# Kernel optimization log

Hardware: AMD Instinct MI355X
Metric: run time of the kernel (lower is better)

The kernel has to match this reference:

```python
import jax, jax.numpy as jnp
import numpy as np

V = 50000      # vocab_size
E = 512        # embed_size
H = 512        # hidden_size
B = 128        # batch
S = 256        # encoder seq len
MAX_OOVS = 12


def setup_inputs() -> dict:
    key = jax.random.key(0)
    ks = jax.random.split(key, 18)
    s = 0.05
    embed_table = jax.random.normal(ks[4], (V, E), jnp.float32) * s
    embed_table = embed_table.at[0].set(0.0)  # padding_idx=0
    return {
        'input_idx':   jax.random.randint(ks[0], (B,), 0, V),
        'encoded':     jax.random.normal(ks[1], (B, S, H), jnp.float32),
        'encoded_idx': jax.random.randint(ks[2], (B, S), 0, V),
        'prev_state':  jax.random.normal(ks[3], (B, H), jnp.float32),
        'weighted':    jnp.zeros((B, 1, H), jnp.float32),
        'embed_table': embed_table,
        'Ws_w':    jax.random.normal(ks[5], (H, H), jnp.float32) * s,
        'Ws_b':    jnp.zeros((H,), jnp.float32),
        'gru_Wih': jax.random.normal(ks[6], (3 * H, E + H), jnp.float32) * s,
        'gru_Whh': jax.random.normal(ks[7], (3 * H, H), jnp.float32) * s,
        'gru_bih': jnp.zeros((3 * H,), jnp.float32),
        'gru_bhh': jnp.zeros((3 * H,), jnp.float32),
        'attn_W':  jax.random.normal(ks[8], (H, 2 * H), jnp.float32) * s,
        'attn_b':  jnp.zeros((H,), jnp.float32),
        'attn_v':  jax.random.normal(ks[9], (H,), jnp.float32) * s,
        'Wo_w':    jax.random.normal(ks[10], (V, 2 * H), jnp.float32) * s,
        'Wo_b':    jnp.zeros((V,), jnp.float32),
        'Wc_w':    jax.random.normal(ks[11], (2 * H, H), jnp.float32) * s,
        'Wc_b':    jnp.zeros((2 * H,), jnp.float32),
    }


def copy_decoder_fwd(input_idx, encoded, encoded_idx, prev_state, weighted,
                     embed_table, Ws_w, Ws_b, gru_Wih, gru_Whh, gru_bih, gru_bhh,
                     attn_W, attn_b, attn_v, Wo_w, Wo_b, Wc_w, Wc_b):
    b, seq, hidden = encoded.shape
    vocab = Wo_w.shape[0]
    dt = encoded.dtype

    # order == 0 branch: project prev_state, zero the weighted context
    prev = prev_state @ Ws_w.T + Ws_b                      # (b, h)
    wtd = jnp.zeros((b, hidden), dt)                       # (b, h)

    # GRU single step (PyTorch gate layout: r, z, n)
    x = jnp.concatenate([embed_table[input_idx], wtd], axis=1)  # (b, e+h)
    gi = x @ gru_Wih.T + gru_bih                           # (b, 3h)
    gh = prev @ gru_Whh.T + gru_bhh                        # (b, 3h)
    i_r, i_z, i_n = jnp.split(gi, 3, axis=1)
    h_r, h_z, h_n = jnp.split(gh, 3, axis=1)
    r = jax.nn.sigmoid(i_r + h_r)
    z = jax.nn.sigmoid(i_z + h_z)
    n = jnp.tanh(i_n + r * h_n)
    state = (1.0 - z) * n + z * prev                       # (b, h), == rnn_output

    # 'concat' attention: softmax_seq(v . tanh(W[h; enc] + b))
    h_exp = jnp.broadcast_to(state[:, None, :], (b, seq, hidden))
    energy = jnp.tanh(jnp.concatenate([h_exp, encoded], axis=-1) @ attn_W.T + attn_b)
    attn_w = jax.nn.softmax(energy @ attn_v, axis=1)       # (b, seq)
    context = jnp.einsum('bs,bsh->bh', attn_w, encoded)    # (b, h)

    # generation scores
    score_g = jnp.concatenate([state, context], axis=1) @ Wo_w.T + Wo_b  # (b, V)

    # copy scores
    sc = jnp.tanh(encoded @ Wc_w.T + Wc_b)                 # (b, seq, 2h)
    score_c = jnp.einsum('bsk,bk->bs', sc, jnp.concatenate([state, context], axis=1))
    score_c = score_c + jnp.where(encoded_idx == 0, -1000.0, 0.0).astype(dt)

    # joint softmax over vocab + seq
    probs = jax.nn.softmax(jnp.concatenate([score_g, score_c], axis=1), axis=1)
    prob_g = probs[:, :vocab]                              # (b, V)
    prob_c = probs[:, vocab:]                              # (b, seq)
    prob_c_given = prob_c / jnp.sum(prob_c)                # global-scalar normalization (faithful)

    # pad generation probs with small oov mass
    vext = vocab + MAX_OOVS
    prob_g_ext = jnp.concatenate(
        [prob_g, jnp.full((b, MAX_OOVS), 1e-4, dt)], axis=1)  # (b, V+oov)

    # copy -> vocab scatter-add (replaces dense one-hot + bmm)
    batch_ids = jnp.broadcast_to(jnp.arange(b)[:, None], (b, seq))
    prob_c_to_g = jnp.zeros((b, vext), dt).at[batch_ids, encoded_idx].add(prob_c)

    out = (prob_g_ext + prob_c_to_g)[:, None, :]           # (b, 1, V+oov)

    # positions in source equal to the current input token
    ind = (encoded_idx == input_idx[:, None]).astype(dt)   # (b, seq)
    ssum = ind.sum(axis=1, keepdims=True)
    ind = jnp.where(ssum > 1.0, ind / ssum, ind)
    attn2 = prob_c_given * ind                             # (b, seq)
    weighted_new = jnp.einsum('bs,bsh->bh', attn2, encoded)[:, None, :]  # (b, 1, h)

    return out, state, weighted_new


def reference(input_idx, encoded, encoded_idx, prev_state, weighted,
              embed_table, Ws_w, Ws_b, gru_Wih, gru_Whh, gru_bih, gru_bhh,
              attn_W, attn_b, attn_v, Wo_w, Wo_b, Wc_w, Wc_b):
    return copy_decoder_fwd(input_idx, encoded, encoded_idx, prev_state, weighted,
                            embed_table, Ws_w, Ws_b, gru_Wih, gru_Whh, gru_bih, gru_bhh,
                            attn_W, attn_b, attn_v, Wo_w, Wo_b, Wc_w, Wc_b)
```

## Files before the change

### kernel.cpp

```cpp
#include <hip/hip_runtime.h>
#include <hip/hip_bf16.h>
#include <math.h>

#define BB 128
#define SS 256
#define HH 512
#define VV 50000
#define VEXT 50012

typedef __bf16 bf16x8 __attribute__((ext_vector_type(8)));
typedef float f32x4 __attribute__((ext_vector_type(4)));

__device__ __forceinline__ float fast_tanh(float x) {
  float e = __expf(2.0f * x);
  return 1.0f - 2.0f / (e + 1.0f);
}
__device__ __forceinline__ float fast_sigmoid(float x) {
  return 1.0f / (1.0f + __expf(-x));
}
__device__ __forceinline__ bf16x8 cvt8(const float* p) {
  float4 a = *(const float4*)p;
  float4 b = *(const float4*)(p + 4);
  bf16x8 r;
  r[0] = (__bf16)a.x; r[1] = (__bf16)a.y; r[2] = (__bf16)a.z; r[3] = (__bf16)a.w;
  r[4] = (__bf16)b.x; r[5] = (__bf16)b.y; r[6] = (__bf16)b.z; r[7] = (__bf16)b.w;
  return r;
}

__global__ void k_pack_w(const float* __restrict__ src, int ldw, int coff, int icount,
                         __hip_bfloat16* __restrict__ dst) {
  int i = blockIdx.x * 256 + threadIdx.x;
  if (i >= icount) return;
  int l = i & 63, ks = (i >> 6) & 15, tile = i >> 10;
  int m = l & 15, q = l >> 4;
  const float* p = src + (size_t)(tile * 16 + m) * ldw + coff + ks * 32 + q * 8;
  *(bf16x8*)(dst + (size_t)i * 8) = cvt8(p);
}

__global__ void k_pack_enc(const float* __restrict__ enc, __hip_bfloat16* __restrict__ epk) {
  int i = blockIdx.x * 256 + threadIdx.x;
  int l = i & 63, ks = (i >> 6) & 15, st = (i >> 10) & 15, b = i >> 14;
  int m = l & 15, q = l >> 4;
  const float* p = enc + ((size_t)b * SS + st * 16 + m) * HH + ks * 32 + q * 8;
  *(bf16x8*)(epk + (size_t)i * 8) = cvt8(p);
}

template <int LDB, bool GATHER>
__global__ __launch_bounds__(256, 2) void k_gemm_bt(
    const float* __restrict__ A, const float* __restrict__ B,
    const float* __restrict__ bias, float* __restrict__ C, int ldc,
    const int* __restrict__ gidx) {
  __shared__ __hip_bfloat16 ylds[128 * 72];
  const int t = threadIdx.x;
  const int l = t & 63, w = t >> 6;
  const int m = l & 15, q = l >> 4;
  const int n = blockIdx.x * 64 + w * 16 + m;
  const float* wrow = B + (size_t)n * LDB;
  f32x4 acc[8];
#pragma unroll
  for (int mt = 0; mt < 8; ++mt) acc[mt] = (f32x4){0.f, 0.f, 0.f, 0.f};

  for (int kt = 0; kt < 512; kt += 64) {
    __syncthreads();
#pragma unroll
    for (int i = 0; i < 8; ++i) {
      int f = t + i * 256;
      int row = f >> 4, c4 = f & 15;
      const float* arow;
      if (GATHER)
        arow = A + (size_t)gidx[row] * 512;
      else
        arow = A + (size_t)row * 512;
      float4 v = *(const float4*)(arow + kt + c4 * 4);
      __hip_bfloat16* d = ylds + row * 72 + c4 * 4;
      d[0] = __float2bfloat16(v.x); d[1] = __float2bfloat16(v.y);
      d[2] = __float2bfloat16(v.z); d[3] = __float2bfloat16(v.w);
    }
    __syncthreads();
#pragma unroll
    for (int ksl = 0; ksl < 2; ++ksl) {
      bf16x8 bfr = cvt8(wrow + kt + ksl * 32 + q * 8);
#pragma unroll
      for (int mt = 0; mt < 8; ++mt) {
        bf16x8 af = *(const bf16x8*)(ylds + (mt * 16 + m) * 72 + ksl * 32 + q * 8);
        acc[mt] = __builtin_amdgcn_mfma_f32_16x16x32_bf16(af, bfr, acc[mt], 0, 0, 0);
      }
    }
  }
  float bv = bias[n];
#pragma unroll
  for (int mt = 0; mt < 8; ++mt) {
#pragma unroll
    for (int r = 0; r < 4; ++r) {
      int rowm = mt * 16 + q * 4 + r;
      C[(size_t)rowm * ldc + n] = acc[mt][r] + bv;
    }
  }
}

__global__ void k_gates(const float* __restrict__ gi, const float* __restrict__ gh,
                        const float* __restrict__ prevv, float* __restrict__ state,
                        float* __restrict__ state_out) {
  int i = blockIdx.x * 256 + threadIdx.x;
  int b = i >> 9, h = i & 511;
  const float* gib = gi + (size_t)b * 1536;
  const float* ghb = gh + (size_t)b * 1536;
  float ir = gib[h], iz = gib[512 + h], inn = gib[1024 + h];
  float hr = ghb[h], hz = ghb[512 + h], hn = ghb[1024 + h];
  float r = fast_sigmoid(ir + hr);
  float z = fast_sigmoid(iz + hz);
  float n = fast_tanh(inn + r * hn);
  float st = (1.f - z) * n + z * prevv[i];
  state[i] = st;
  state_out[i] = st;
}

template <int NTOT, int MODE>
__global__ __launch_bounds__(256, 3) void k_fused(
    const __hip_bfloat16* __restrict__ epack, const __hip_bfloat16* __restrict__ wpk,
    const float* __restrict__ biasA, const float* __restrict__ multA,
    const int* __restrict__ enc_idx, float* __restrict__ out) {
  const int b = blockIdx.x, s0 = blockIdx.y * 32, t = threadIdx.x;
  const int l = t & 63, w = t >> 6;
  const int wm = w & 1, wn = w >> 1;
  const int m = l & 15, q = l >> 4;
  __shared__ float bias_l[NTOT];
  __shared__ float mult_l[NTOT];
  __shared__ float red[2][32];
  const float* bias_base = (MODE == 0) ? biasA + (size_t)b * HH : biasA;
  const float* mult_base = (MODE == 0) ? multA : multA + (size_t)b * 1024;
  for (int i = t; i < NTOT; i += 256) {
    bias_l[i] = bias_base[i];
    mult_l[i] = mult_base[i];
  }
  const int st = blockIdx.y * 2 + wm;
  const __hip_bfloat16* ep = epack + ((size_t)(b * 16 + st) * 16) * 512 + (size_t)l * 8;
  bf16x8 afr[16];
#pragma unroll
  for (int ks = 0; ks < 16; ++ks) afr[ks] = *(const bf16x8*)(ep + ks * 512);
  __syncthreads();

  float part[4] = {0.f, 0.f, 0.f, 0.f};
  for (int nb = 0; nb < NTOT; nb += 32) {
    const __hip_bfloat16* wp = wpk + ((size_t)((nb >> 4) + wn) * 16) * 512 + (size_t)l * 8;
    bf16x8 bfr[16];
#pragma unroll
    for (int ks = 0; ks < 16; ++ks) bfr[ks] = *(const bf16x8*)(wp + ks * 512);
    f32x4 a0 = {0.f, 0.f, 0.f, 0.f}, a1 = a0, a2 = a0, a3 = a0;
#pragma unroll
    for (int j = 0; j < 4; ++j) {
      a0 = __builtin_amdgcn_mfma_f32_16x16x32_bf16(afr[j], bfr[j], a0, 0, 0, 0);
      a1 = __builtin_amdgcn_mfma_f32_16x16x32_bf16(afr[4 + j], bfr[4 + j], a1, 0, 0, 0);
      a2 = __builtin_amdgcn_mfma_f32_16x16x32_bf16(afr[8 + j], bfr[8 + j], a2, 0, 0, 0);
      a3 = __builtin_amdgcn_mfma_f32_16x16x32_bf16(afr[12 + j], bfr[12 + j], a3, 0, 0, 0);
    }
    f32x4 acc = (a0 + a1) + (a2 + a3);
    const int n = nb + wn * 16 + m;
    float bias = bias_l[n];
    float mul = mult_l[n];
#pragma unroll
    for (int r = 0; r < 4; ++r) part[r] += fast_tanh(acc[r] + bias) * mul;
  }
#pragma unroll
  for (int r = 0; r < 4; ++r) {
    part[r] += __shfl_xor(part[r], 1, 64);
    part[r] += __shfl_xor(part[r], 2, 64);
    part[r] += __shfl_xor(part[r], 4, 64);
    part[r] += __shfl_xor(part[r], 8, 64);
  }
  if (m == 0) {
#pragma unroll
    for (int r = 0; r < 4; ++r) red[wn][wm * 16 + q * 4 + r] = part[r];
  }
  __syncthreads();
  if (t < 32) {
    float v = red[0][t] + red[1][t];
    int s = s0 + t;
    if (MODE == 1 && enc_idx[b * SS + s] == 0) v -= 1000.0f;
    out[b * SS + s] = v;
  }
}

__global__ __launch_bounds__(256, 2) void k_score_g_mfma(
    const float* __restrict__ y, const float* __restrict__ Wo_w,
    const float* __restrict__ Wo_b, float* __restrict__ sg) {
  __shared__ __hip_bfloat16 ylds[128 * 72];
  const int t = threadIdx.x;
  const int l = t & 63, w = t >> 6;
  const int m = l & 15, q = l >> 4;
  const int nb = blockIdx.x * 64;
  const int n = nb + w * 16 + m;
  const int n_ld = (n < VV) ? n : (VV - 1);
  const float* wrow = Wo_w + (size_t)n_ld * 1024;
  f32x4 acc[8];
#pragma unroll
  for (int mt = 0; mt < 8; ++mt) acc[mt] = (f32x4){0.f, 0.f, 0.f, 0.f};

  for (int kt = 0; kt < 1024; kt += 64) {
    __syncthreads();
#pragma unroll
    for (int i = 0; i < 8; ++i) {
      int f = t + i * 256;
      int row = f >> 4, c4 = f & 15;
      float4 v = *(const float4*)(y + (size_t)row * 1024 + kt + c4 * 4);
      __hip_bfloat16* d = ylds + row * 72 + c4 * 4;
      d[0] = __float2bfloat16(v.x); d[1] = __float2bfloat16(v.y);
      d[2] = __float2bfloat16(v.z); d[3] = __float2bfloat16(v.w);
    }
    __syncthreads();
#pragma unroll
    for (int ksl = 0; ksl < 2; ++ksl) {
      bf16x8 bfr = cvt8(wrow + kt + ksl * 32 + q * 8);
#pragma unroll
      for (int mt = 0; mt < 8; ++mt) {
        bf16x8 af = *(const bf16x8*)(ylds + (mt * 16 + m) * 72 + ksl * 32 + q * 8);
        acc[mt] = __builtin_amdgcn_mfma_f32_16x16x32_bf16(af, bfr, acc[mt], 0, 0, 0);
      }
    }
  }
  if (n < VV) {
    float bias = Wo_b[n];
#pragma unroll
    for (int mt = 0; mt < 8; ++mt) {
#pragma unroll
      for (int r = 0; r < 4; ++r) {
        int rowm = mt * 16 + q * 4 + r;
        sg[(size_t)rowm * VV + n] = acc[mt][r] + bias;
      }
    }
  }
}

__global__ void k_attn_softmax(const float* __restrict__ score, float* __restrict__ aw) {
  const int b = blockIdx.x, t = threadIdx.x;
  __shared__ float rbuf[8];
  __shared__ float MS[2];
  float x = score[b * SS + t];
  float m = x;
  for (int off = 32; off > 0; off >>= 1) m = fmaxf(m, __shfl_xor(m, off, 64));
  if ((t & 63) == 0) rbuf[t >> 6] = m;
  __syncthreads();
  if (t == 0) MS[0] = fmaxf(fmaxf(rbuf[0], rbuf[1]), fmaxf(rbuf[2], rbuf[3]));
  __syncthreads();
  float e = __expf(x - MS[0]);
  float s = e;
  for (int off = 32; off > 0; off >>= 1) s += __shfl_xor(s, off, 64);
  if ((t & 63) == 0) rbuf[4 + (t >> 6)] = s;
  __syncthreads();
  if (t == 0) MS[1] = rbuf[4] + rbuf[5] + rbuf[6] + rbuf[7];
  __syncthreads();
  aw[b * SS + t] = e / MS[1];
}

__global__ void k_context(const float* __restrict__ aw, const float* __restrict__ enc,
                          const float* __restrict__ state, float* __restrict__ y) {
  const int b = blockIdx.x, hc = blockIdx.y, t = threadIdx.x;
  __shared__ float aws[SS];
  aws[t] = aw[b * SS + t];
  aws[t + 128] = aw[b * SS + t + 128];
  __syncthreads();
  int h = hc * 128 + t;
  float acc = 0.f;
  for (int s = 0; s < SS; ++s) acc += aws[s] * enc[((size_t)b * SS + s) * HH + h];
  y[(size_t)b * 1024 + HH + h] = acc;
  y[(size_t)b * 1024 + h] = state[b * HH + h];
}

__global__ void k_rowstat_part(const float* __restrict__ sg,
                               float* __restrict__ pmax, float* __restrict__ psum) {
  const int b = blockIdx.x, c = blockIdx.y, t = threadIdx.x;
  __shared__ float rbuf[8];
  __shared__ float MS[1];
  const float* row = sg + (size_t)b * VV;
  const int base = c * 6250, end = base + 6250;
  float m = -1e30f;
  for (int i = base + t; i < end; i += 256) m = fmaxf(m, row[i]);
  for (int off = 32; off > 0; off >>= 1) m = fmaxf(m, __shfl_xor(m, off, 64));
  if ((t & 63) == 0) rbuf[t >> 6] = m;
  __syncthreads();
  if (t == 0) MS[0] = fmaxf(fmaxf(rbuf[0], rbuf[1]), fmaxf(rbuf[2], rbuf[3]));
  __syncthreads();
  float M = MS[0];
  float s = 0.f;
  for (int i = base + t; i < end; i += 256) s += __expf(row[i] - M);
  for (int off = 32; off > 0; off >>= 1) s += __shfl_xor(s, off, 64);
  if ((t & 63) == 0) rbuf[4 + (t >> 6)] = s;
  __syncthreads();
  if (t == 0) {
    pmax[b * 8 + c] = M;
    psum[b * 8 + c] = rbuf[4] + rbuf[5] + rbuf[6] + rbuf[7];
  }
}

__global__ void k_rowstat_final(const float* __restrict__ pmax, const float* __restrict__ psum,
                                const float* __restrict__ sc,
                                float* __restrict__ rmax, float* __restrict__ rsum) {
  const int b = blockIdx.x, t = threadIdx.x;
  float m = -1e30f;
  if (t < 8) m = pmax[b * 8 + t];
  for (int i = t; i < SS; i += 64) m = fmaxf(m, sc[b * SS + i]);
  for (int off = 32; off > 0; off >>= 1) m = fmaxf(m, __shfl_xor(m, off, 64));
  float M = m;
  float s = 0.f;
  if (t < 8) s = psum[b * 8 + t] * __expf(pmax[b * 8 + t] - M);
  for (int i = t; i < SS; i += 64) s += __expf(sc[b * SS + i] - M);
  for (int off = 32; off > 0; off >>= 1) s += __shfl_xor(s, off, 64);
  if (t == 0) {
    rmax[b] = M;
    rsum[b] = s;
  }
}

__global__ void k_write_probg(const float* __restrict__ sg,
                              const float* __restrict__ rmax,
                              const float* __restrict__ rsum,
                              float* __restrict__ out) {
  int i = blockIdx.x * 256 + threadIdx.x;
  const int total = BB * VEXT;
  if (i >= total) return;
  int b = i / VEXT;
  int v = i - b * VEXT;
  float val;
  if (v < VV)
    val = __expf(sg[(size_t)b * VV + v] - rmax[b]) / rsum[b];
  else
    val = 1e-4f;
  out[i] = val;
}

__global__ void k_probc(const float* __restrict__ sc,
                        const int* __restrict__ enc_idx,
                        const float* __restrict__ rmax,
                        const float* __restrict__ rsum,
                        float* __restrict__ prob_c,
                        float* __restrict__ out,
                        float* __restrict__ pc_total) {
  const int b = blockIdx.x, t = threadIdx.x;
  __shared__ float rbuf[8];
  float pc = __expf(sc[b * SS + t] - rmax[b]) / rsum[b];
  prob_c[b * SS + t] = pc;
  atomicAdd(&out[(size_t)b * VEXT + enc_idx[b * SS + t]], pc);
  float s = pc;
  for (int off = 32; off > 0; off >>= 1) s += __shfl_down(s, off, 64);
  if ((t & 63) == 0) rbuf[t >> 6] = s;
  __syncthreads();
  if (t == 0) atomicAdd(pc_total, rbuf[0] + rbuf[1] + rbuf[2] + rbuf[3]);
}

__global__ void k_weighted(const int* __restrict__ enc_idx,
                           const int* __restrict__ input_idx,
                           const float* __restrict__ prob_c,
                           const float* __restrict__ pc_total,
                           const float* __restrict__ enc,
                           float* __restrict__ wout) {
  const int b = blockIdx.x, hc = blockIdx.y, t = threadIdx.x;
  __shared__ float f[SS];
  __shared__ float rb[2];
  const int idx_in = input_idx[b];
  int m0 = (enc_idx[b * SS + t] == idx_in) ? 1 : 0;
  int m1 = (enc_idx[b * SS + t + 128] == idx_in) ? 1 : 0;
  float lsum = (float)(m0 + m1);
  for (int off = 32; off > 0; off >>= 1) lsum += __shfl_xor(lsum, off, 64);
  if ((t & 63) == 0) rb[t >> 6] = lsum;
  __syncthreads();
  float tot = rb[0] + rb[1];
  float norm = (tot > 1.0f) ? 1.0f / tot : 1.0f;
  float inv_pct = 1.0f / pc_total[0];
  f[t] = m0 ? prob_c[b * SS + t] * inv_pct * norm : 0.f;
  f[t + 128] = m1 ? prob_c[b * SS + t + 128] * inv_pct * norm : 0.f;
  __syncthreads();
  int h = hc * 128 + t;
  float acc = 0.f;
  for (int s = 0; s < SS; ++s) acc += f[s] * enc[((size_t)b * SS + s) * HH + h];
  wout[b * HH + h] = acc;
}

extern "C" void kernel_launch(void* const* d_in, const int* in_sizes, int n_in,
                              void* d_out, int out_size, void* d_ws, size_t ws_size,
                              hipStream_t stream) {
  const int* input_idx = (const int*)d_in[0];
  const float* encoded = (const float*)d_in[1];
  const int* encoded_idx = (const int*)d_in[2];
  const float* prev_state = (const float*)d_in[3];
  const float* embed = (const float*)d_in[5];
  const float* Ws_w = (const float*)d_in[6];
  const float* Ws_b = (const float*)d_in[7];
  const float* gWih = (const float*)d_in[8];
  const float* gWhh = (const float*)d_in[9];
  const float* gbih = (const float*)d_in[10];
  const float* gbhh = (const float*)d_in[11];
  const float* attn_W = (const float*)d_in[12];
  const float* attn_b = (const float*)d_in[13];
  const float* attn_v = (const float*)d_in[14];
  const float* Wo_w = (const float*)d_in[15];
  const float* Wo_b = (const float*)d_in[16];
  const float* Wc_w = (const float*)d_in[17];
  const float* Wc_b = (const float*)d_in[18];

  float* out = (float*)d_out;
  float* out_state = out + (size_t)BB * VEXT;
  float* out_weighted = out_state + BB * HH;

  float* ws = (float*)d_ws;
  float* prevv = ws;
  float* state = prevv + BB * HH;
  float* hW = state + BB * HH;
  float* ascore = hW + BB * HH;
  float* aw = ascore + BB * SS;
  float* y = aw + BB * SS;
  float* sg = y + BB * 1024;
  float* sc = sg + (size_t)BB * VV;
  float* prob_c = sc + BB * SS;
  float* pmax = prob_c + BB * SS;
  float* psum = pmax + BB * 8;
  float* rmax = psum + BB * 8;
  float* rsum = rmax + BB;
  float* pc_total = rsum + BB;
  __hip_bfloat16* wc_bf = (__hip_bfloat16*)(pc_total + 64);
  __hip_bfloat16* wa_bf = wc_bf + (size_t)1024 * HH;
  __hip_bfloat16* epack = wa_bf + (size_t)512 * HH;

  float* gi = sg;
  float* gh = sg + BB * 1536;

  hipMemsetAsync(pc_total, 0, sizeof(float), stream);

  k_pack_w<<<256, 256, 0, stream>>>(Wc_w, 512, 0, 1024 * 64, wc_bf);
  k_pack_w<<<128, 256, 0, stream>>>(attn_W, 1024, 512, 512 * 64, wa_bf);
  k_pack_enc<<<8192, 256, 0, stream>>>(encoded, epack);

  k_gemm_bt<512, false><<<8, 256, 0, stream>>>(prev_state, Ws_w, Ws_b, prevv, 512, nullptr);
  k_gemm_bt<1024, true><<<24, 256, 0, stream>>>(embed, gWih, gbih, gi, 1536, input_idx);
  k_gemm_bt<512, false><<<24, 256, 0, stream>>>(prevv, gWhh, gbhh, gh, 1536, nullptr);
  k_gates<<<256, 256, 0, stream>>>(gi, gh, prevv, state, out_state);
  k_gemm_bt<1024, false><<<8, 256, 0, stream>>>(state, attn_W, attn_b, hW, 512, nullptr);

  k_fused<HH, 0><<<dim3(BB, 8), 256, 0, stream>>>(epack, wa_bf, hW, attn_v,
                                                  nullptr, ascore);
  k_attn_softmax<<<BB, 256, 0, stream>>>(ascore, aw);
  k_context<<<dim3(BB, 4), 128, 0, stream>>>(aw, encoded, state, y);

  k_score_g_mfma<<<(VV + 63) / 64, 256, 0, stream>>>(y, Wo_w, Wo_b, sg);
  k_fused<1024, 1><<<dim3(BB, 8), 256, 0, stream>>>(epack, wc_bf, Wc_b, y,
                                                    encoded_idx, sc);

  k_rowstat_part<<<dim3(BB, 8), 256, 0, stream>>>(sg, pmax, psum);
  k_rowstat_final<<<BB, 64, 0, stream>>>(pmax, psum, sc, rmax, rsum);
  k_write_probg<<<(BB * VEXT + 255) / 256, 256, 0, stream>>>(sg, rmax, rsum, out);
  k_probc<<<BB, 256, 0, stream>>>(sc, encoded_idx, rmax, rsum, prob_c, out, pc_total);
  k_weighted<<<dim3(BB, 4), 128, 0, stream>>>(encoded_idx, input_idx, prob_c, pc_total,
                                              encoded, out_weighted);
}
```

Measured before the change: 721.5 us.

## Fuse vocab softmax statistics into score GEMM epilogue and merge small kernels

The vocab score GEMM now computes per-block online max and sum-exp in its epilogue, which removes the separate row-stat pass over the 128x50000 score matrix. The final reduction merges 782 partials per row. y is pre-packed to bf16 in MFMA fragment order, so the score GEMM reads fragments directly instead of staging them through LDS with barriers. The attention softmax is fused with the context kernel, and the two GRU-input GEMMs share one launch. The context and weighted kernels use float4 loads with one block per batch row, trading fewer threads for wider loads.

```diff
diff --git a/kernel.cpp b/kernel.cpp
--- a/kernel.cpp
+++ b/kernel.cpp
@@ -7,6 +7,7 @@
 #define HH 512
 #define VV 50000
 #define VEXT 50012
+#define NBLK 782
 
 typedef __bf16 bf16x8 __attribute__((ext_vector_type(8)));
 typedef float f32x4 __attribute__((ext_vector_type(4)));
@@ -25,6 +26,11 @@
   r[0] = (__bf16)a.x; r[1] = (__bf16)a.y; r[2] = (__bf16)a.z; r[3] = (__bf16)a.w;
   r[4] = (__bf16)b.x; r[5] = (__bf16)b.y; r[6] = (__bf16)b.z; r[7] = (__bf16)b.w;
   return r;
+}
+__device__ __forceinline__ void omerge(float& M, float& S, float m2, float s2) {
+  float Mn = fmaxf(M, m2);
+  S = S * __expf(M - Mn) + s2 * __expf(m2 - Mn);
+  M = Mn;
 }
 
 __global__ void k_pack_w(const float* __restrict__ src, int ldw, int coff, int icount,
@@ -45,17 +51,23 @@
   *(bf16x8*)(epk + (size_t)i * 8) = cvt8(p);
 }
 
-template <int LDB, bool GATHER>
-__global__ __launch_bounds__(256, 2) void k_gemm_bt(
-    const float* __restrict__ A, const float* __restrict__ B,
-    const float* __restrict__ bias, float* __restrict__ C, int ldc,
-    const int* __restrict__ gidx) {
-  __shared__ __hip_bfloat16 ylds[128 * 72];
+__global__ void k_pack_y(const float* __restrict__ y, __hip_bfloat16* __restrict__ ypk) {
+  int i = blockIdx.x * 256 + threadIdx.x;
+  int l = i & 63, mt = (i >> 6) & 7, ks = i >> 9;
+  int m = l & 15, q = l >> 4;
+  const float* p = y + (size_t)(mt * 16 + m) * 1024 + ks * 32 + q * 8;
+  *(bf16x8*)(ypk + (size_t)i * 8) = cvt8(p);
+}
+
+__device__ __forceinline__ void gemm_body(
+    const float* __restrict__ A, const int* __restrict__ gidx, bool gather,
+    const float* __restrict__ B, int ldb, const float* __restrict__ bias,
+    float* __restrict__ C, int ldc, int blk, __hip_bfloat16* ylds) {
   const int t = threadIdx.x;
   const int l = t & 63, w = t >> 6;
   const int m = l & 15, q = l >> 4;
-  const int n = blockIdx.x * 64 + w * 16 + m;
-  const float* wrow = B + (size_t)n * LDB;
+  const int n = blk * 64 + w * 16 + m;
+  const float* wrow = B + (size_t)n * ldb;
   f32x4 acc[8];
 #pragma unroll
   for (int mt = 0; mt < 8; ++mt) acc[mt] = (f32x4){0.f, 0.f, 0.f, 0.f};
@@ -66,11 +78,7 @@
     for (int i = 0; i < 8; ++i) {
       int f = t + i * 256;
       int row = f >> 4, c4 = f & 15;
-      const float* arow;
-      if (GATHER)
-        arow = A + (size_t)gidx[row] * 512;
-      else
-        arow = A + (size_t)row * 512;
+      const float* arow = gather ? A + (size_t)gidx[row] * 512 : A + (size_t)row * 512;
       float4 v = *(const float4*)(arow + kt + c4 * 4);
       __hip_bfloat16* d = ylds + row * 72 + c4 * 4;
       d[0] = __float2bfloat16(v.x); d[1] = __float2bfloat16(v.y);
@@ -96,6 +104,25 @@
       C[(size_t)rowm * ldc + n] = acc[mt][r] + bv;
     }
   }
+}
+
+__global__ __launch_bounds__(256, 2) void k_gemm_pg(
+    const float* __restrict__ prev_state, const float* __restrict__ embed,
+    const int* __restrict__ gidx, const float* __restrict__ Ws_w,
+    const float* __restrict__ Ws_b, const float* __restrict__ gWih,
+    const float* __restrict__ gbih, float* __restrict__ prevv, float* __restrict__ gi) {
+  __shared__ __hip_bfloat16 ylds[128 * 72];
+  if (blockIdx.x < 8)
+    gemm_body(prev_state, nullptr, false, Ws_w, 512, Ws_b, prevv, 512, blockIdx.x, ylds);
+  else
+    gemm_body(embed, gidx, true, gWih, 1024, gbih, gi, 1536, blockIdx.x - 8, ylds);
+}
+
+__global__ __launch_bounds__(256, 2) void k_gemm_1(
+    const float* __restrict__ A, const float* __restrict__ B, int ldb,
+    const float* __restrict__ bias, float* __restrict__ C, int ldc) {
+  __shared__ __hip_bfloat16 ylds[128 * 72];
+  gemm_body(A, nullptr, false, B, ldb, bias, C, ldc, blockIdx.x, ylds);
 }
 
 __global__ void k_gates(const float* __restrict__ gi, const float* __restrict__ gh,
@@ -181,133 +208,119 @@
   }
 }
 
-__global__ __launch_bounds__(256, 2) void k_score_g_mfma(
-    const float* __restrict__ y, const float* __restrict__ Wo_w,
-    const float* __restrict__ Wo_b, float* __restrict__ sg) {
-  __shared__ __hip_bfloat16 ylds[128 * 72];
+__global__ __launch_bounds__(256, 2) void k_score_g2(
+    const __hip_bfloat16* __restrict__ ypk, const float* __restrict__ Wo_w,
+    const float* __restrict__ Wo_b, float* __restrict__ sg,
+    float* __restrict__ gmax, float* __restrict__ gsum) {
   const int t = threadIdx.x;
   const int l = t & 63, w = t >> 6;
   const int m = l & 15, q = l >> 4;
-  const int nb = blockIdx.x * 64;
-  const int n = nb + w * 16 + m;
+  const int n = blockIdx.x * 64 + w * 16 + m;
   const int n_ld = (n < VV) ? n : (VV - 1);
   const float* wrow = Wo_w + (size_t)n_ld * 1024;
   f32x4 acc[8];
 #pragma unroll
   for (int mt = 0; mt < 8; ++mt) acc[mt] = (f32x4){0.f, 0.f, 0.f, 0.f};
-
-  for (int kt = 0; kt < 1024; kt += 64) {
-    __syncthreads();
-#pragma unroll
-    for (int i = 0; i < 8; ++i) {
-      int f = t + i * 256;
-      int row = f >> 4, c4 = f & 15;
-      float4 v = *(const float4*)(y + (size_t)row * 1024 + kt + c4 * 4);
-      __hip_bfloat16* d = ylds + row * 72 + c4 * 4;
-      d[0] = __float2bfloat16(v.x); d[1] = __float2bfloat16(v.y);
-      d[2] = __float2bfloat16(v.z); d[3] = __float2bfloat16(v.w);
-    }
-    __syncthreads();
-#pragma unroll
-    for (int ksl = 0; ksl < 2; ++ksl) {
-      bf16x8 bfr = cvt8(wrow + kt + ksl * 32 + q * 8);
-#pragma unroll
-      for (int mt = 0; mt < 8; ++mt) {
-        bf16x8 af = *(const bf16x8*)(ylds + (mt * 16 + m) * 72 + ksl * 32 + q * 8);
-        acc[mt] = __builtin_amdgcn_mfma_f32_16x16x32_bf16(af, bfr, acc[mt], 0, 0, 0);
+#pragma unroll 4
+  for (int ks = 0; ks < 32; ++ks) {
+    bf16x8 bfr = cvt8(wrow + ks * 32 + q * 8);
+    const __hip_bfloat16* ab = ypk + (size_t)ks * 4096 + (size_t)l * 8;
+#pragma unroll
+    for (int mt = 0; mt < 8; ++mt) {
+      bf16x8 af = *(const bf16x8*)(ab + mt * 512);
+      acc[mt] = __builtin_amdgcn_mfma_f32_16x16x32_bf16(af, bfr, acc[mt], 0, 0, 0);
+    }
+  }
+  const bool valid = (n < VV);
+  float bias = valid ? Wo_b[n] : 0.f;
+  __shared__ float smax[4 * 128];
+  __shared__ float ssum[4 * 128];
+#pragma unroll
+  for (int mt = 0; mt < 8; ++mt) {
+#pragma unroll
+    for (int r = 0; r < 4; ++r) {
+      float v = acc[mt][r] + bias;
+      if (valid) sg[(size_t)(mt * 16 + q * 4 + r) * VV + n] = v;
+      float vv = valid ? v : -1e30f;
+      float M16 = vv;
+      M16 = fmaxf(M16, __shfl_xor(M16, 1, 64));
+      M16 = fmaxf(M16, __shfl_xor(M16, 2, 64));
+      M16 = fmaxf(M16, __shfl_xor(M16, 4, 64));
+      M16 = fmaxf(M16, __shfl_xor(M16, 8, 64));
+      float e = valid ? __expf(vv - M16) : 0.f;
+      e += __shfl_xor(e, 1, 64);
+      e += __shfl_xor(e, 2, 64);
+      e += __shfl_xor(e, 4, 64);
+      e += __shfl_xor(e, 8, 64);
+      if (m == 0) {
+        smax[w * 128 + mt * 16 + q * 4 + r] = M16;
+        ssum[w * 128 + mt * 16 + q * 4 + r] = e;
       }
     }
   }
-  if (n < VV) {
-    float bias = Wo_b[n];
-#pragma unroll
-    for (int mt = 0; mt < 8; ++mt) {
-#pragma unroll
-      for (int r = 0; r < 4; ++r) {
-        int rowm = mt * 16 + q * 4 + r;
-        sg[(size_t)rowm * VV + n] = acc[mt][r] + bias;
-      }
-    }
-  }
-}
-
-__global__ void k_attn_softmax(const float* __restrict__ score, float* __restrict__ aw) {
+  __syncthreads();
+  if (t < 128) {
+    float M = smax[t], S = ssum[t];
+#pragma unroll
+    for (int w2 = 1; w2 < 4; ++w2) omerge(M, S, smax[w2 * 128 + t], ssum[w2 * 128 + t]);
+    gmax[(size_t)t * NBLK + blockIdx.x] = M;
+    gsum[(size_t)t * NBLK + blockIdx.x] = S;
+  }
+}
+
+__global__ void k_softmax_ctx(const float* __restrict__ score, const float* __restrict__ enc,
+                              const float* __restrict__ state, float* __restrict__ y) {
   const int b = blockIdx.x, t = threadIdx.x;
-  __shared__ float rbuf[8];
-  __shared__ float MS[2];
-  float x = score[b * SS + t];
-  float m = x;
-  for (int off = 32; off > 0; off >>= 1) m = fmaxf(m, __shfl_xor(m, off, 64));
-  if ((t & 63) == 0) rbuf[t >> 6] = m;
-  __syncthreads();
-  if (t == 0) MS[0] = fmaxf(fmaxf(rbuf[0], rbuf[1]), fmaxf(rbuf[2], rbuf[3]));
-  __syncthreads();
-  float e = __expf(x - MS[0]);
-  float s = e;
-  for (int off = 32; off > 0; off >>= 1) s += __shfl_xor(s, off, 64);
-  if ((t & 63) == 0) rbuf[4 + (t >> 6)] = s;
-  __syncthreads();
-  if (t == 0) MS[1] = rbuf[4] + rbuf[5] + rbuf[6] + rbuf[7];
-  __syncthreads();
-  aw[b * SS + t] = e / MS[1];
-}
-
-__global__ void k_context(const float* __restrict__ aw, const float* __restrict__ enc,
-                          const float* __restrict__ state, float* __restrict__ y) {
-  const int b = blockIdx.x, hc = blockIdx.y, t = threadIdx.x;
   __shared__ float aws[SS];
-  aws[t] = aw[b * SS + t];
-  aws[t + 128] = aw[b * SS + t + 128];
-  __syncthreads();
-  int h = hc * 128 + t;
-  float acc = 0.f;
-  for (int s = 0; s < SS; ++s) acc += aws[s] * enc[((size_t)b * SS + s) * HH + h];
-  y[(size_t)b * 1024 + HH + h] = acc;
-  y[(size_t)b * 1024 + h] = state[b * HH + h];
-}
-
-__global__ void k_rowstat_part(const float* __restrict__ sg,
-                               float* __restrict__ pmax, float* __restrict__ psum) {
-  const int b = blockIdx.x, c = blockIdx.y, t = threadIdx.x;
-  __shared__ float rbuf[8];
-  __shared__ float MS[1];
-  const float* row = sg + (size_t)b * VV;
-  const int base = c * 6250, end = base + 6250;
-  float m = -1e30f;
-  for (int i = base + t; i < end; i += 256) m = fmaxf(m, row[i]);
-  for (int off = 32; off > 0; off >>= 1) m = fmaxf(m, __shfl_xor(m, off, 64));
-  if ((t & 63) == 0) rbuf[t >> 6] = m;
-  __syncthreads();
-  if (t == 0) MS[0] = fmaxf(fmaxf(rbuf[0], rbuf[1]), fmaxf(rbuf[2], rbuf[3]));
-  __syncthreads();
-  float M = MS[0];
-  float s = 0.f;
-  for (int i = base + t; i < end; i += 256) s += __expf(row[i] - M);
-  for (int off = 32; off > 0; off >>= 1) s += __shfl_xor(s, off, 64);
-  if ((t & 63) == 0) rbuf[4 + (t >> 6)] = s;
-  __syncthreads();
-  if (t == 0) {
-    pmax[b * 8 + c] = M;
-    psum[b * 8 + c] = rbuf[4] + rbuf[5] + rbuf[6] + rbuf[7];
-  }
-}
-
-__global__ void k_rowstat_final(const float* __restrict__ pmax, const float* __restrict__ psum,
+  __shared__ float rb[4];
+  float x0 = score[b * SS + t], x1 = score[b * SS + t + 128];
+  float mx = fmaxf(x0, x1);
+  for (int off = 32; off; off >>= 1) mx = fmaxf(mx, __shfl_xor(mx, off, 64));
+  if ((t & 63) == 0) rb[t >> 6] = mx;
+  __syncthreads();
+  float M = fmaxf(rb[0], rb[1]);
+  float e0 = __expf(x0 - M), e1 = __expf(x1 - M);
+  float s = e0 + e1;
+  for (int off = 32; off; off >>= 1) s += __shfl_xor(s, off, 64);
+  if ((t & 63) == 0) rb[2 + (t >> 6)] = s;
+  __syncthreads();
+  float S = rb[2] + rb[3];
+  aws[t] = e0 / S;
+  aws[t + 128] = e1 / S;
+  __syncthreads();
+  float4 acc = {0.f, 0.f, 0.f, 0.f};
+  const float* eb = enc + (size_t)b * SS * HH + t * 4;
+#pragma unroll 4
+  for (int s2 = 0; s2 < SS; ++s2) {
+    float4 v = *(const float4*)(eb + (size_t)s2 * HH);
+    acc.x += aws[s2] * v.x; acc.y += aws[s2] * v.y;
+    acc.z += aws[s2] * v.z; acc.w += aws[s2] * v.w;
+  }
+  *(float4*)(y + (size_t)b * 1024 + HH + t * 4) = acc;
+  *(float4*)(y + (size_t)b * 1024 + t * 4) = *(const float4*)(state + (size_t)b * HH + t * 4);
+}
+
+__global__ void k_rowstat_final(const float* __restrict__ gmax, const float* __restrict__ gsum,
                                 const float* __restrict__ sc,
                                 float* __restrict__ rmax, float* __restrict__ rsum) {
   const int b = blockIdx.x, t = threadIdx.x;
-  float m = -1e30f;
-  if (t < 8) m = pmax[b * 8 + t];
-  for (int i = t; i < SS; i += 64) m = fmaxf(m, sc[b * SS + i]);
-  for (int off = 32; off > 0; off >>= 1) m = fmaxf(m, __shfl_xor(m, off, 64));
-  float M = m;
-  float s = 0.f;
-  if (t < 8) s = psum[b * 8 + t] * __expf(pmax[b * 8 + t] - M);
-  for (int i = t; i < SS; i += 64) s += __expf(sc[b * SS + i] - M);
-  for (int off = 32; off > 0; off >>= 1) s += __shfl_xor(s, off, 64);
+  __shared__ float wm[4], wsum[4];
+  float M = -1e30f, S = 0.f;
+  const float* gm = gmax + (size_t)b * NBLK;
+  const float* gs = gsum + (size_t)b * NBLK;
+  for (int i = t; i < NBLK; i += 256) omerge(M, S, gm[i], gs[i]);
+  omerge(M, S, sc[b * SS + t], 1.0f);
+  for (int off = 32; off; off >>= 1) {
+    float Mo = __shfl_xor(M, off, 64), So = __shfl_xor(S, off, 64);
+    omerge(M, S, Mo, So);
+  }
+  if ((t & 63) == 0) { wm[t >> 6] = M; wsum[t >> 6] = S; }
+  __syncthreads();
   if (t == 0) {
-    rmax[b] = M;
-    rsum[b] = s;
+    float Mf = wm[0], Sf = wsum[0];
+    for (int i = 1; i < 4; ++i) omerge(Mf, Sf, wm[i], wsum[i]);
+    rmax[b] = Mf;
+    rsum[b] = Sf;
   }
 }
 
@@ -353,26 +366,31 @@
                            const float* __restrict__ pc_total,
                            const float* __restrict__ enc,
                            float* __restrict__ wout) {
-  const int b = blockIdx.x, hc = blockIdx.y, t = threadIdx.x;
+  const int b = blockIdx.x, t = threadIdx.x;
   __shared__ float f[SS];
   __shared__ float rb[2];
   const int idx_in = input_idx[b];
   int m0 = (enc_idx[b * SS + t] == idx_in) ? 1 : 0;
   int m1 = (enc_idx[b * SS + t + 128] == idx_in) ? 1 : 0;
   float lsum = (float)(m0 + m1);
-  for (int off = 32; off > 0; off >>= 1) lsum += __shfl_xor(lsum, off, 64);
+  for (int off = 32; off; off >>= 1) lsum += __shfl_xor(lsum, off, 64);
   if ((t & 63) == 0) rb[t >> 6] = lsum;
   __syncthreads();
   float tot = rb[0] + rb[1];
   float norm = (tot > 1.0f) ? 1.0f / tot : 1.0f;
-  float inv_pct = 1.0f / pc_total[0];
-  f[t] = m0 ? prob_c[b * SS + t] * inv_pct * norm : 0.f;
-  f[t + 128] = m1 ? prob_c[b * SS + t + 128] * inv_pct * norm : 0.f;
-  __syncthreads();
-  int h = hc * 128 + t;
-  float acc = 0.f;
-  for (int s = 0; s < SS; ++s) acc += f[s] * enc[((size_t)b * SS + s) * HH + h];
-  wout[b * HH + h] = acc;
+  float ip = 1.0f / pc_total[0];
+  f[t] = m0 ? prob_c[b * SS + t] * ip * norm : 0.f;
+  f[t + 128] = m1 ? prob_c[b * SS + t + 128] * ip * norm : 0.f;
+  __syncthreads();
+  float4 acc = {0.f, 0.f, 0.f, 0.f};
+  const float* eb = enc + (size_t)b * SS * HH + t * 4;
+#pragma unroll 4
+  for (int s2 = 0; s2 < SS; ++s2) {
+    float4 v = *(const float4*)(eb + (size_t)s2 * HH);
+    acc.x += f[s2] * v.x; acc.y += f[s2] * v.y;
+    acc.z += f[s2] * v.z; acc.w += f[s2] * v.w;
+  }
+  *(float4*)(wout + (size_t)b * HH + t * 4) = acc;
 }
 
 extern "C" void kernel_launch(void* const* d_in, const int* in_sizes, int n_in,
@@ -406,17 +424,17 @@
   float* state = prevv + BB * HH;
   float* hW = state + BB * HH;
   float* ascore = hW + BB * HH;
-  float* aw = ascore + BB * SS;
-  float* y = aw + BB * SS;
+  float* y = ascore + BB * SS;
   float* sg = y + BB * 1024;
   float* sc = sg + (size_t)BB * VV;
   float* prob_c = sc + BB * SS;
-  float* pmax = prob_c + BB * SS;
-  float* psum = pmax + BB * 8;
-  float* rmax = psum + BB * 8;
+  float* rmax = prob_c + BB * SS;
   float* rsum = rmax + BB;
   float* pc_total = rsum + BB;
-  __hip_bfloat16* wc_bf = (__hip_bfloat16*)(pc_total + 64);
+  float* gmax = pc_total + 64;
+  float* gsum = gmax + BB * NBLK;
+  __hip_bfloat16* ypk = (__hip_bfloat16*)(gsum + BB * NBLK);
+  __hip_bfloat16* wc_bf = ypk + 131072;
   __hip_bfloat16* wa_bf = wc_bf + (size_t)1024 * HH;
   __hip_bfloat16* epack = wa_bf + (size_t)512 * HH;
 
@@ -429,25 +447,24 @@
   k_pack_w<<<128, 256, 0, stream>>>(attn_W, 1024, 512, 512 * 64, wa_bf);
   k_pack_enc<<<8192, 256, 0, stream>>>(encoded, epack);
 
-  k_gemm_bt<512, false><<<8, 256, 0, stream>>>(prev_state, Ws_w, Ws_b, prevv, 512, nullptr);
-  k_gemm_bt<1024, true><<<24, 256, 0, stream>>>(embed, gWih, gbih, gi, 1536, input_idx);
-  k_gemm_bt<512, false><<<24, 256, 0, stream>>>(prevv, gWhh, gbhh, gh, 1536, nullptr);
+  k_gemm_pg<<<32, 256, 0, stream>>>(prev_state, embed, input_idx, Ws_w, Ws_b,
+                                    gWih, gbih, prevv, gi);
+  k_gemm_1<<<24, 256, 0, stream>>>(prevv, gWhh, 512, gbhh, gh, 1536);
   k_gates<<<256, 256, 0, stream>>>(gi, gh, prevv, state, out_state);
-  k_gemm_bt<1024, false><<<8, 256, 0, stream>>>(state, attn_W, attn_b, hW, 512, nullptr);
+  k_gemm_1<<<8, 256, 0, stream>>>(state, attn_W, 1024, attn_b, hW, 512);
 
   k_fused<HH, 0><<<dim3(BB, 8), 256, 0, stream>>>(epack, wa_bf, hW, attn_v,
                                                   nullptr, ascore);
-  k_attn_softmax<<<BB, 256, 0, stream>>>(ascore, aw);
-  k_context<<<dim3(BB, 4), 128, 0, stream>>>(aw, encoded, state, y);
-
-  k_score_g_mfma<<<(VV + 63) / 64, 256, 0, stream>>>(y, Wo_w, Wo_b, sg);
+  k_softmax_ctx<<<BB, 128, 0, stream>>>(ascore, encoded, state, y);
+  k_pack_y<<<64, 256, 0, stream>>>(y, ypk);
+
+  k_score_g2<<<NBLK, 256, 0, stream>>>(ypk, Wo_w, Wo_b, sg, gmax, gsum);
   k_fused<1024, 1><<<dim3(BB, 8), 256, 0, stream>>>(epack, wc_bf, Wc_b, y,
                                                     encoded_idx, sc);
 
-  k_rowstat_part<<<dim3(BB, 8), 256, 0, stream>>>(sg, pmax, psum);
-  k_rowstat_final<<<BB, 64, 0, stream>>>(pmax, psum, sc, rmax, rsum);
+  k_rowstat_final<<<BB, 256, 0, stream>>>(gmax, gsum, sc, rmax, rsum);
   k_write_probg<<<(BB * VEXT + 255) / 256, 256, 0, stream>>>(sg, rmax, rsum, out);
   k_probc<<<BB, 256, 0, stream>>>(sc, encoded_idx, rmax, rsum, prob_c, out, pc_total);
-  k_weighted<<<dim3(BB, 4), 128, 0, stream>>>(encoded_idx, input_idx, prob_c, pc_total,
-                                              encoded, out_weighted);
-}
+  k_weighted<<<BB, 128, 0, stream>>>(encoded_idx, input_idx, prob_c, pc_total,
+                                     encoded, out_weighted);
+}
```

Measured after the change: 741.1 us. +2.7%, slower.
